# Optimization experiments

Hardware: AMD Instinct MI355X
Metric: run time of the kernel (lower is better)

Reference implementation:

```python
import jax, jax.numpy as jnp
import numpy as np

N_Q = 32      # questions per batch
N_DOCS = 8    # docs per question (positive first)
Q_LEN = 32    # query tokens
D_LEN = 200   # doc tokens
DIM = 128     # ColBERT embedding dim


def setup_inputs() -> dict:
    key = jax.random.key(0)
    k1, k2 = jax.random.split(key)
    hq = jax.random.normal(k1, (N_Q, Q_LEN, DIM), dtype=jnp.float32)
    hd = jax.random.normal(k2, (N_Q * N_DOCS, D_LEN, DIM), dtype=jnp.float32)
    return {"hq": hq, "hd": hd}


def reference(hq, hd):
    # ColBERT maxsim: [n, m, q, d] token-level scores
    scores = jnp.einsum("nqh,mdh->nmqd", hq, hd)
    # max over doc tokens, mean over query tokens -> [n, m]
    score_matrix = jnp.max(scores, axis=-1).mean(axis=-1)

    n, m = score_matrix.shape
    n_docs = m // n
    # positive doc is the first in each group: targets = [0, n_docs, 2*n_docs, ...]
    targets = jnp.arange(0, m, n_docs)
    logp = jax.nn.log_softmax(score_matrix, axis=-1)
    loss = -jnp.mean(jnp.take_along_axis(logp, targets[:, None], axis=1))
    return score_matrix, loss
```

## Files before the change

kernel.cpp:

```cpp
#include <hip/hip_runtime.h>
#include <hip/hip_bf16.h>
#include <math.h>

typedef short short8 __attribute__((ext_vector_type(8)));
typedef float f32x4 __attribute__((ext_vector_type(4)));

#define NQ 32
#define NDOCS 8
#define QLEN 32
#define DLEN 200
#define DIM 128
#define MD 256
#define ROWB 256

__device__ __forceinline__ short f2bf(float x) {
    union { float f; unsigned u; } v; v.f = x;
    unsigned r = v.u + 0x7FFFu + ((v.u >> 16) & 1u);
    return (short)(r >> 16);
}

__device__ __forceinline__ short8 cvt8(float4 f0, float4 f1) {
    short8 o;
    o[0] = f2bf(f0.x); o[1] = f2bf(f0.y); o[2] = f2bf(f0.z); o[3] = f2bf(f0.w);
    o[4] = f2bf(f1.x); o[5] = f2bf(f1.y); o[6] = f2bf(f1.z); o[7] = f2bf(f1.w);
    return o;
}

__device__ __forceinline__ void writeChunk(char* lds, int c, float4 f0, float4 f1) {
    int row = c >> 4, kc = c & 15;
    int byte = row * ROWB + ((kc * 16) ^ ((row & 7) << 4));
    *reinterpret_cast<short8*>(&lds[byte]) = cvt8(f0, f1);
}

__global__ __launch_bounds__(256, 2) void colbert_scores(const float* __restrict__ hq,
                                                         const float* __restrict__ hd,
                                                         float* __restrict__ out) {
    __shared__ char lds[208 * ROWB];
    const int tid = threadIdx.x;
    const int b = blockIdx.x;
    const int m = b & 255, qo = b >> 8;
    const int wid = tid >> 6, lane = tid & 63;
    const int lg = lane >> 4, lr = lane & 15;
    const int n0 = qo * 8 + wid * 2;

    const float4* src4 = reinterpret_cast<const float4*>(hd + (size_t)m * (DLEN * DIM));
    #pragma unroll
    for (int i = 0; i < 12; ++i) {
        int c = tid + i * 256;
        float4 f0 = src4[c * 2], f1 = src4[c * 2 + 1];
        writeChunk(lds, c, f0, f1);
    }
    if (tid < 128) {
        int c = 3072 + tid;
        float4 f0 = src4[c * 2], f1 = src4[c * 2 + 1];
        writeChunk(lds, c, f0, f1);
    }

    short8 Bq[2][2][4];
    #pragma unroll
    for (int nn = 0; nn < 2; ++nn)
        #pragma unroll
        for (int qt = 0; qt < 2; ++qt)
            #pragma unroll
            for (int s = 0; s < 4; ++s) {
                const float4* p = reinterpret_cast<const float4*>(
                    hq + (size_t)((n0 + nn) * QLEN + qt * 16 + lr) * DIM + s * 32 + lg * 8);
                Bq[nn][qt][s] = cvt8(p[0], p[1]);
            }

    __syncthreads();

    int va[4];
    #pragma unroll
    for (int s = 0; s < 4; ++s)
        va[s] = lr * ROWB + ((s * 64 + lg * 16) ^ ((lr & 7) << 4));

    float qmax[2][2];
    #pragma unroll
    for (int nn = 0; nn < 2; ++nn)
        #pragma unroll
        for (int qt = 0; qt < 2; ++qt) qmax[nn][qt] = -INFINITY;

#define STEP(DT, MASKED)                                                          \
    {                                                                             \
        f32x4 a00 = {0,0,0,0}, a01 = {0,0,0,0}, a10 = {0,0,0,0}, a11 = {0,0,0,0}; \
        _Pragma("unroll")                                                         \
        for (int s = 0; s < 4; ++s) {                                             \
            short8 A_ = *reinterpret_cast<const short8*>(&lds[va[s] + (DT) * 4096]); \
            a00 = __builtin_amdgcn_mfma_f32_16x16x32_bf16(A_, Bq[0][0][s], a00, 0, 0, 0); \
            a01 = __builtin_amdgcn_mfma_f32_16x16x32_bf16(A_, Bq[0][1][s], a01, 0, 0, 0); \
            a10 = __builtin_amdgcn_mfma_f32_16x16x32_bf16(A_, Bq[1][0][s], a10, 0, 0, 0); \
            a11 = __builtin_amdgcn_mfma_f32_16x16x32_bf16(A_, Bq[1][1][s], a11, 0, 0, 0); \
        }                                                                         \
        if (!(MASKED) || lg < 2) {                                                \
            qmax[0][0] = fmaxf(qmax[0][0], fmaxf(fmaxf(a00[0], a00[1]), fmaxf(a00[2], a00[3]))); \
            qmax[0][1] = fmaxf(qmax[0][1], fmaxf(fmaxf(a01[0], a01[1]), fmaxf(a01[2], a01[3]))); \
            qmax[1][0] = fmaxf(qmax[1][0], fmaxf(fmaxf(a10[0], a10[1]), fmaxf(a10[2], a10[3]))); \
            qmax[1][1] = fmaxf(qmax[1][1], fmaxf(fmaxf(a11[0], a11[1]), fmaxf(a11[2], a11[3]))); \
        }                                                                         \
    }

    #pragma unroll
    for (int dt = 0; dt < 12; ++dt) STEP(dt, false);
    STEP(12, true);
#undef STEP

    #pragma unroll
    for (int off = 16; off <= 32; off <<= 1)
        #pragma unroll
        for (int nn = 0; nn < 2; ++nn)
            #pragma unroll
            for (int qt = 0; qt < 2; ++qt)
                qmax[nn][qt] = fmaxf(qmax[nn][qt], __shfl_xor(qmax[nn][qt], off, 64));

    float s0 = qmax[0][0] + qmax[0][1];
    float s1 = qmax[1][0] + qmax[1][1];
    #pragma unroll
    for (int off = 1; off <= 8; off <<= 1) {
        s0 += __shfl_xor(s0, off, 64);
        s1 += __shfl_xor(s1, off, 64);
    }
    if (lane == 0) {
        out[(size_t)n0 * MD + m] = s0 * (1.0f / 32.0f);
        out[(size_t)(n0 + 1) * MD + m] = s1 * (1.0f / 32.0f);
    }
}

__global__ __launch_bounds__(256) void colbert_loss(const float* __restrict__ scores,
                                                    float* __restrict__ loss_out) {
    __shared__ float terms[NQ];
    const int tid = threadIdx.x;
    const int wid = tid >> 6, lane = tid & 63;
    for (int n = wid; n < NQ; n += 4) {
        const float* row = scores + n * MD;
        float v0 = row[lane], v1 = row[64 + lane], v2 = row[128 + lane], v3 = row[192 + lane];
        float mx = fmaxf(fmaxf(v0, v1), fmaxf(v2, v3));
        #pragma unroll
        for (int off = 1; off < 64; off <<= 1) mx = fmaxf(mx, __shfl_xor(mx, off, 64));
        float s = expf(v0 - mx) + expf(v1 - mx) + expf(v2 - mx) + expf(v3 - mx);
        #pragma unroll
        for (int off = 1; off < 64; off <<= 1) s += __shfl_xor(s, off, 64);
        if (lane == 0) terms[n] = (mx + logf(s)) - row[n * NDOCS];
    }
    __syncthreads();
    if (tid == 0) {
        float acc = 0.f;
        #pragma unroll
        for (int n = 0; n < NQ; ++n) acc += terms[n];
        loss_out[0] = acc * (1.0f / NQ);
    }
}

extern "C" void kernel_launch(void* const* d_in, const int* in_sizes, int n_in,
                              void* d_out, int out_size, void* d_ws, size_t ws_size,
                              hipStream_t stream) {
    const float* hq = (const float*)d_in[0];
    const float* hd = (const float*)d_in[1];
    float* out = (float*)d_out;

    colbert_scores<<<1024, 256, 0, stream>>>(hq, hd, out);
    colbert_loss<<<1, 256, 0, stream>>>(out, out + NQ * MD);
}
```

Baseline: 39.71 us.

## Load each doc once per block and compute all queries with 8 waves

The grid shrinks from 1024 blocks (doc × query-octet) to 256 blocks of 512 threads, one per doc. Each doc is converted into LDS once instead of four times, and each wave now handles 4 queries instead of 2. This cuts redundant global reads and bf16 conversion of hd, but there are fewer blocks (256 across the CUs) and more registers per thread (8 accumulators, 32 Bq fragments), which can limit occupancy. Padding rows 200-207 of LDS are now zero-filled.

```diff
diff --git a/kernel.cpp b/kernel.cpp
--- a/kernel.cpp
+++ b/kernel.cpp
@@ -32,21 +32,20 @@
     *reinterpret_cast<short8*>(&lds[byte]) = cvt8(f0, f1);
 }
 
-__global__ __launch_bounds__(256, 2) void colbert_scores(const float* __restrict__ hq,
+__global__ __launch_bounds__(512, 2) void colbert_scores(const float* __restrict__ hq,
                                                          const float* __restrict__ hd,
                                                          float* __restrict__ out) {
     __shared__ char lds[208 * ROWB];
     const int tid = threadIdx.x;
-    const int b = blockIdx.x;
-    const int m = b & 255, qo = b >> 8;
+    const int m = blockIdx.x;
     const int wid = tid >> 6, lane = tid & 63;
     const int lg = lane >> 4, lr = lane & 15;
-    const int n0 = qo * 8 + wid * 2;
+    const int n0 = wid * 4;
 
     const float4* src4 = reinterpret_cast<const float4*>(hd + (size_t)m * (DLEN * DIM));
     #pragma unroll
-    for (int i = 0; i < 12; ++i) {
-        int c = tid + i * 256;
+    for (int i = 0; i < 6; ++i) {
+        int c = tid + i * 512;
         float4 f0 = src4[c * 2], f1 = src4[c * 2 + 1];
         writeChunk(lds, c, f0, f1);
     }
@@ -54,11 +53,13 @@
         int c = 3072 + tid;
         float4 f0 = src4[c * 2], f1 = src4[c * 2 + 1];
         writeChunk(lds, c, f0, f1);
+        float4 z = {0.f, 0.f, 0.f, 0.f};
+        writeChunk(lds, 3200 + tid, z, z);
     }
 
-    short8 Bq[2][2][4];
+    short8 Bq[4][2][4];
     #pragma unroll
-    for (int nn = 0; nn < 2; ++nn)
+    for (int nn = 0; nn < 4; ++nn)
         #pragma unroll
         for (int qt = 0; qt < 2; ++qt)
             #pragma unroll
@@ -75,28 +76,37 @@
     for (int s = 0; s < 4; ++s)
         va[s] = lr * ROWB + ((s * 64 + lg * 16) ^ ((lr & 7) << 4));
 
-    float qmax[2][2];
+    float qmax[4][2];
     #pragma unroll
-    for (int nn = 0; nn < 2; ++nn)
+    for (int nn = 0; nn < 4; ++nn)
         #pragma unroll
         for (int qt = 0; qt < 2; ++qt) qmax[nn][qt] = -INFINITY;
 
 #define STEP(DT, MASKED)                                                          \
     {                                                                             \
-        f32x4 a00 = {0,0,0,0}, a01 = {0,0,0,0}, a10 = {0,0,0,0}, a11 = {0,0,0,0}; \
+        f32x4 acc[4][2];                                                          \
+        _Pragma("unroll")                                                         \
+        for (int nn = 0; nn < 4; ++nn)                                            \
+            _Pragma("unroll")                                                     \
+            for (int qt = 0; qt < 2; ++qt) acc[nn][qt] = (f32x4){0.f,0.f,0.f,0.f};\
         _Pragma("unroll")                                                         \
         for (int s = 0; s < 4; ++s) {                                             \
             short8 A_ = *reinterpret_cast<const short8*>(&lds[va[s] + (DT) * 4096]); \
-            a00 = __builtin_amdgcn_mfma_f32_16x16x32_bf16(A_, Bq[0][0][s], a00, 0, 0, 0); \
-            a01 = __builtin_amdgcn_mfma_f32_16x16x32_bf16(A_, Bq[0][1][s], a01, 0, 0, 0); \
-            a10 = __builtin_amdgcn_mfma_f32_16x16x32_bf16(A_, Bq[1][0][s], a10, 0, 0, 0); \
-            a11 = __builtin_amdgcn_mfma_f32_16x16x32_bf16(A_, Bq[1][1][s], a11, 0, 0, 0); \
+            _Pragma("unroll")                                                     \
+            for (int nn = 0; nn < 4; ++nn)                                        \
+                _Pragma("unroll")                                                 \
+                for (int qt = 0; qt < 2; ++qt)                                    \
+                    acc[nn][qt] = __builtin_amdgcn_mfma_f32_16x16x32_bf16(        \
+                        A_, Bq[nn][qt][s], acc[nn][qt], 0, 0, 0);                 \
         }                                                                         \
         if (!(MASKED) || lg < 2) {                                                \
-            qmax[0][0] = fmaxf(qmax[0][0], fmaxf(fmaxf(a00[0], a00[1]), fmaxf(a00[2], a00[3]))); \
-            qmax[0][1] = fmaxf(qmax[0][1], fmaxf(fmaxf(a01[0], a01[1]), fmaxf(a01[2], a01[3]))); \
-            qmax[1][0] = fmaxf(qmax[1][0], fmaxf(fmaxf(a10[0], a10[1]), fmaxf(a10[2], a10[3]))); \
-            qmax[1][1] = fmaxf(qmax[1][1], fmaxf(fmaxf(a11[0], a11[1]), fmaxf(a11[2], a11[3]))); \
+            _Pragma("unroll")                                                     \
+            for (int nn = 0; nn < 4; ++nn)                                        \
+                _Pragma("unroll")                                                 \
+                for (int qt = 0; qt < 2; ++qt)                                    \
+                    qmax[nn][qt] = fmaxf(qmax[nn][qt],                            \
+                        fmaxf(fmaxf(acc[nn][qt][0], acc[nn][qt][1]),              \
+                              fmaxf(acc[nn][qt][2], acc[nn][qt][3])));            \
         }                                                                         \
     }
 
@@ -108,21 +118,17 @@
     #pragma unroll
     for (int off = 16; off <= 32; off <<= 1)
         #pragma unroll
-        for (int nn = 0; nn < 2; ++nn)
+        for (int nn = 0; nn < 4; ++nn)
             #pragma unroll
             for (int qt = 0; qt < 2; ++qt)
                 qmax[nn][qt] = fmaxf(qmax[nn][qt], __shfl_xor(qmax[nn][qt], off, 64));
 
-    float s0 = qmax[0][0] + qmax[0][1];
-    float s1 = qmax[1][0] + qmax[1][1];
     #pragma unroll
-    for (int off = 1; off <= 8; off <<= 1) {
-        s0 += __shfl_xor(s0, off, 64);
-        s1 += __shfl_xor(s1, off, 64);
-    }
-    if (lane == 0) {
-        out[(size_t)n0 * MD + m] = s0 * (1.0f / 32.0f);
-        out[(size_t)(n0 + 1) * MD + m] = s1 * (1.0f / 32.0f);
+    for (int nn = 0; nn < 4; ++nn) {
+        float s = qmax[nn][0] + qmax[nn][1];
+        #pragma unroll
+        for (int off = 1; off <= 8; off <<= 1) s += __shfl_xor(s, off, 64);
+        if (lane == 0) out[(size_t)(n0 + nn) * MD + m] = s * (1.0f / 32.0f);
     }
 }
 
@@ -158,6 +164,6 @@
     const float* hd = (const float*)d_in[1];
     float* out = (float*)d_out;
 
-    colbert_scores<<<1024, 256, 0, stream>>>(hq, hd, out);
+    colbert_scores<<<MD, 512, 0, stream>>>(hq, hd, out);
     colbert_loss<<<1, 256, 0, stream>>>(out, out + NQ * MD);
 }
```

After: 44.29 us. +11.5%, slower.

## Double-buffer doc tiles in LDS to overlap global loads with MFMA

Applied to the files above, without the earlier changes.

Replaces the single upfront load of the whole 200-token document into LDS with a double-buffered loop that stages 32-token chunks and prefetches the next chunk into registers while computing MFMAs on the current one. This cuts LDS usage from about 52KB to 16KB per block, which may allow more blocks per CU, and overlaps global memory latency with compute. It adds a barrier per chunk and a non-unrolled loop. It also swaps the manual bf16 rounding for the HIP __float2bfloat16 intrinsic.

```diff
diff --git a/kernel.cpp b/kernel.cpp
--- a/kernel.cpp
+++ b/kernel.cpp
@@ -13,29 +13,25 @@
 #define MD 256
 #define ROWB 256
 
-__device__ __forceinline__ short f2bf(float x) {
-    union { float f; unsigned u; } v; v.f = x;
-    unsigned r = v.u + 0x7FFFu + ((v.u >> 16) & 1u);
-    return (short)(r >> 16);
+__device__ __forceinline__ short8 cvt8(float4 f0, float4 f1) {
+    union { __hip_bfloat16 h[8]; short8 s; } u;
+    u.h[0] = __float2bfloat16(f0.x); u.h[1] = __float2bfloat16(f0.y);
+    u.h[2] = __float2bfloat16(f0.z); u.h[3] = __float2bfloat16(f0.w);
+    u.h[4] = __float2bfloat16(f1.x); u.h[5] = __float2bfloat16(f1.y);
+    u.h[6] = __float2bfloat16(f1.z); u.h[7] = __float2bfloat16(f1.w);
+    return u.s;
 }
 
-__device__ __forceinline__ short8 cvt8(float4 f0, float4 f1) {
-    short8 o;
-    o[0] = f2bf(f0.x); o[1] = f2bf(f0.y); o[2] = f2bf(f0.z); o[3] = f2bf(f0.w);
-    o[4] = f2bf(f1.x); o[5] = f2bf(f1.y); o[6] = f2bf(f1.z); o[7] = f2bf(f1.w);
-    return o;
-}
-
-__device__ __forceinline__ void writeChunk(char* lds, int c, float4 f0, float4 f1) {
+__device__ __forceinline__ void writeChunk(char* buf, int c, float4 f0, float4 f1) {
     int row = c >> 4, kc = c & 15;
     int byte = row * ROWB + ((kc * 16) ^ ((row & 7) << 4));
-    *reinterpret_cast<short8*>(&lds[byte]) = cvt8(f0, f1);
+    *reinterpret_cast<short8*>(&buf[byte]) = cvt8(f0, f1);
 }
 
 __global__ __launch_bounds__(256, 2) void colbert_scores(const float* __restrict__ hq,
                                                          const float* __restrict__ hd,
                                                          float* __restrict__ out) {
-    __shared__ char lds[208 * ROWB];
+    __shared__ char lds[2][32 * ROWB];
     const int tid = threadIdx.x;
     const int b = blockIdx.x;
     const int m = b & 255, qo = b >> 8;
@@ -44,17 +40,6 @@
     const int n0 = qo * 8 + wid * 2;
 
     const float4* src4 = reinterpret_cast<const float4*>(hd + (size_t)m * (DLEN * DIM));
-    #pragma unroll
-    for (int i = 0; i < 12; ++i) {
-        int c = tid + i * 256;
-        float4 f0 = src4[c * 2], f1 = src4[c * 2 + 1];
-        writeChunk(lds, c, f0, f1);
-    }
-    if (tid < 128) {
-        int c = 3072 + tid;
-        float4 f0 = src4[c * 2], f1 = src4[c * 2 + 1];
-        writeChunk(lds, c, f0, f1);
-    }
 
     short8 Bq[2][2][4];
     #pragma unroll
@@ -68,6 +53,12 @@
                 Bq[nn][qt][s] = cvt8(p[0], p[1]);
             }
 
+    {
+        float4 a0 = src4[tid * 2],           a1 = src4[tid * 2 + 1];
+        float4 b0 = src4[(tid + 256) * 2],   b1 = src4[(tid + 256) * 2 + 1];
+        writeChunk(lds[0], tid, a0, a1);
+        writeChunk(lds[0], tid + 256, b0, b1);
+    }
     __syncthreads();
 
     int va[4];
@@ -81,12 +72,12 @@
         #pragma unroll
         for (int qt = 0; qt < 2; ++qt) qmax[nn][qt] = -INFINITY;
 
-#define STEP(DT, MASKED)                                                          \
+#define STEP(BUF, TL, MASKED)                                                     \
     {                                                                             \
         f32x4 a00 = {0,0,0,0}, a01 = {0,0,0,0}, a10 = {0,0,0,0}, a11 = {0,0,0,0}; \
         _Pragma("unroll")                                                         \
         for (int s = 0; s < 4; ++s) {                                             \
-            short8 A_ = *reinterpret_cast<const short8*>(&lds[va[s] + (DT) * 4096]); \
+            short8 A_ = *reinterpret_cast<const short8*>(&(BUF)[va[s] + (TL) * 4096]); \
             a00 = __builtin_amdgcn_mfma_f32_16x16x32_bf16(A_, Bq[0][0][s], a00, 0, 0, 0); \
             a01 = __builtin_amdgcn_mfma_f32_16x16x32_bf16(A_, Bq[0][1][s], a01, 0, 0, 0); \
             a10 = __builtin_amdgcn_mfma_f32_16x16x32_bf16(A_, Bq[1][0][s], a10, 0, 0, 0); \
@@ -100,9 +91,28 @@
         }                                                                         \
     }
 
-    #pragma unroll
-    for (int dt = 0; dt < 12; ++dt) STEP(dt, false);
-    STEP(12, true);
+    #pragma unroll 1
+    for (int g = 0; g < 5; ++g) {
+        const int base = (g + 1) * 512;
+        float4 a0 = src4[(base + tid) * 2],        a1 = src4[(base + tid) * 2 + 1];
+        float4 b0 = src4[(base + tid + 256) * 2],  b1 = src4[(base + tid + 256) * 2 + 1];
+        char* cur = lds[g & 1];
+        STEP(cur, 0, false);
+        STEP(cur, 1, false);
+        char* nxt = lds[(g + 1) & 1];
+        writeChunk(nxt, tid, a0, a1);
+        writeChunk(nxt, tid + 256, b0, b1);
+        __syncthreads();
+    }
+    {
+        float4 a0 = {0,0,0,0}, a1 = {0,0,0,0};
+        if (tid < 128) { a0 = src4[(3072 + tid) * 2]; a1 = src4[(3072 + tid) * 2 + 1]; }
+        STEP(lds[1], 0, false);
+        STEP(lds[1], 1, false);
+        writeChunk(lds[0], tid, a0, a1);
+        __syncthreads();
+    }
+    STEP(lds[0], 0, true);
 #undef STEP
 
     #pragma unroll
```

New measurement: 38.58 us. 1.03x faster.
